# Kernel tuning notes

Hardware: AMD Instinct MI355X
Metric: run time of the kernel (lower is better)

## Reference

```python
import jax, jax.numpy as jnp
import numpy as np

N = 100_000   # nodes
R = 8         # relations (edge types)
E = 100_000   # edges per relation
D_IN = 64
D_OUT = 64


def setup_inputs() -> dict:
    key = jax.random.key(0)
    k1, k2, k3, k4 = jax.random.split(key, 4)
    feat = jax.random.normal(k1, (N, D_IN), dtype=jnp.float32)
    # per-relation weight matrices (nn.ParameterDict in the original)
    weight = jax.random.normal(k2, (R, D_IN, D_OUT), dtype=jnp.float32) / np.sqrt(D_IN).astype(np.float32)
    edge_src = jax.random.randint(k3, (R, E), 0, N)
    edge_dst = jax.random.randint(k4, (R, E), 0, N)
    return {"feat": feat, "weight": weight, "edge_src": edge_src, "edge_dst": edge_dst}


def reference(feat, weight, edge_src, edge_dst):
    # Per-relation: gather src features, dense matmul with that relation's
    # weight, scatter-sum messages into destination nodes; 'sum' across
    # relations (cross-type reducer) collapses into one big scatter-add.
    n = feat.shape[0]
    gathered = feat[edge_src]                            # [R, E, d_in] irregular gather
    msg = jnp.einsum('red,rdf->ref', gathered, weight)   # [R, E, d_out]
    out = jax.ops.segment_sum(
        msg.reshape(-1, msg.shape[-1]),                  # [R*E, d_out]
        edge_dst.reshape(-1),
        num_segments=n,
    )                                                    # [N, d_out]
    return out
```

## Files before the change

### kernel.cpp

```cpp
#include <hip/hip_runtime.h>
#include <hip/hip_bf16.h>


#define WAVES_PER_BLOCK 4
#define EDGES_PER_WAVE 64
#define TILE_E (WAVES_PER_BLOCK * EDGES_PER_WAVE)

__global__ __launch_bounds__(256) void rgcn_edge_kernel(
    const float* __restrict__ feat,
    const float* __restrict__ weight,
    const int*   __restrict__ esrc,
    const int*   __restrict__ edst,
    float*       __restrict__ out,
    int E, int blocksPerRel)
{
    const int t    = threadIdx.x;
    const int wave = t >> 6;
    const int lane = t & 63;

    const int r       = blockIdx.x / blocksPerRel;
    const int tileIdx = blockIdx.x % blocksPerRel;
    const int e0      = tileIdx * TILE_E + wave * EDGES_PER_WAVE;
    if (e0 >= E) return;

    const float* wbase = weight + (size_t)r * 4096 + lane;
    float wreg[64];
    #pragma unroll
    for (int d = 0; d < 64; ++d) wreg[d] = wbase[(size_t)d * 64];

    const int nE = min(EDGES_PER_WAVE, E - e0);
    const int ei = e0 + min(lane, nE - 1);
    const int sv = esrc[(size_t)r * E + ei];
    const int dv = edst[(size_t)r * E + ei];

    float* outl = out + lane;

    for (int i = 0; i < nE; ++i) {
        const int srow = __builtin_amdgcn_readlane(sv, i);
        const int drow = __builtin_amdgcn_readlane(dv, i);

        const float4* xp = (const float4*)(feat + (size_t)srow * 64);
        float a0 = 0.f, a1 = 0.f, a2 = 0.f, a3 = 0.f;
        #pragma unroll
        for (int c = 0; c < 16; ++c) {
            const float4 v = xp[c];
            a0 = fmaf(v.x, wreg[4 * c + 0], a0);
            a1 = fmaf(v.y, wreg[4 * c + 1], a1);
            a2 = fmaf(v.z, wreg[4 * c + 2], a2);
            a3 = fmaf(v.w, wreg[4 * c + 3], a3);
        }
        const float acc = (a0 + a1) + (a2 + a3);

        atomicAdd(outl + (size_t)drow * 64, acc);
    }
}

extern "C" void kernel_launch(void* const* d_in, const int* in_sizes, int n_in,
                              void* d_out, int out_size, void* d_ws, size_t ws_size,
                              hipStream_t stream) {
    const float* feat   = (const float*)d_in[0];
    const float* weight = (const float*)d_in[1];
    const int*   esrc   = (const int*)d_in[2];
    const int*   edst   = (const int*)d_in[3];
    float*       out    = (float*)d_out;

    const int R = in_sizes[1] / (64 * 64);
    const int E = in_sizes[2] / R;

    hipMemsetAsync(d_out, 0, (size_t)out_size * sizeof(float), stream);

    const int blocksPerRel = (E + TILE_E - 1) / TILE_E;
    const dim3 grid(R * blocksPerRel);
    const dim3 block(WAVES_PER_BLOCK * 64);
    rgcn_edge_kernel<<<grid, block, 0, stream>>>(feat, weight, esrc, edst, out,
                                                 E, blocksPerRel);
}
```

Baseline: 263.9 us.

## Bucket edges by destination block and accumulate messages in shared memory

```diff
diff --git a/kernel.cpp b/kernel.cpp
--- a/kernel.cpp
+++ b/kernel.cpp
@@ -2,43 +2,143 @@
 #include <hip/hip_bf16.h>
 
 
-#define WAVES_PER_BLOCK 4
-#define EDGES_PER_WAVE 64
-#define TILE_E (WAVES_PER_BLOCK * EDGES_PER_WAVE)
+#define BUCKET_SHIFT 7
+#define BUCKET_NODES 128
+#define REL_SHIFT 20
 
-__global__ __launch_bounds__(256) void rgcn_edge_kernel(
-    const float* __restrict__ feat,
-    const float* __restrict__ weight,
-    const int*   __restrict__ esrc,
-    const int*   __restrict__ edst,
-    float*       __restrict__ out,
-    int E, int blocksPerRel)
+__global__ __launch_bounds__(256) void k_hist(
+    const int* __restrict__ edst, unsigned* __restrict__ hist, int E, int R)
 {
-    const int t    = threadIdx.x;
-    const int wave = t >> 6;
-    const int lane = t & 63;
+    const int e = blockIdx.x * 256 + threadIdx.x;
+    const int r = blockIdx.y;
+    if (e < E) {
+        const unsigned d = (unsigned)edst[(size_t)r * E + e];
+        atomicAdd(&hist[(d >> BUCKET_SHIFT) * R + r], 1u);
+    }
+}
 
-    const int r       = blockIdx.x / blocksPerRel;
-    const int tileIdx = blockIdx.x % blocksPerRel;
-    const int e0      = tileIdx * TILE_E + wave * EDGES_PER_WAVE;
+__global__ __launch_bounds__(256) void k_scan(
+    const unsigned* __restrict__ hist, unsigned* __restrict__ base,
+    unsigned* __restrict__ cursor, int nbins)
+{
+    __shared__ unsigned psum[256];
+    const int t  = threadIdx.x;
+    const int C  = (nbins + 255) / 256;
+    const int i0 = t * C, i1 = min(i0 + C, nbins);
+    unsigned s = 0;
+    for (int i = i0; i < i1; ++i) s += hist[i];
+    psum[t] = s;
+    __syncthreads();
+    if (t == 0) {
+        unsigned run = 0;
+        for (int i = 0; i < 256; ++i) { unsigned v = psum[i]; psum[i] = run; run += v; }
+        base[nbins] = run;
+    }
+    __syncthreads();
+    unsigned run = psum[t];
+    for (int i = i0; i < i1; ++i) { base[i] = run; cursor[i] = run; run += hist[i]; }
+}
+
+__global__ __launch_bounds__(256) void k_scatter(
+    const int* __restrict__ esrc, const int* __restrict__ edst,
+    unsigned* __restrict__ cursor, uint2* __restrict__ rec, int E, int R)
+{
+    const int e = blockIdx.x * 256 + threadIdx.x;
+    const int r = blockIdx.y;
+    if (e < E) {
+        const size_t idx  = (size_t)r * E + e;
+        const unsigned d  = (unsigned)edst[idx];
+        const unsigned bin  = (d >> BUCKET_SHIFT) * R + r;
+        const unsigned slot = atomicAdd(&cursor[bin], 1u);
+        rec[slot] = make_uint2((unsigned)esrc[idx], d | ((unsigned)r << REL_SHIFT));
+    }
+}
+
+__global__ __launch_bounds__(256) void k_compute(
+    const float* __restrict__ feat, const float* __restrict__ weight,
+    const uint2* __restrict__ rec, const unsigned* __restrict__ base,
+    float* __restrict__ out, int N, int R)
+{
+    __shared__ float acc[BUCKET_NODES * 64];
+    const int t = threadIdx.x, wave = t >> 6, lane = t & 63;
+    const int b = blockIdx.x;
+
+    for (int i = t; i < BUCKET_NODES * 16; i += 256)
+        ((float4*)acc)[i] = make_float4(0.f, 0.f, 0.f, 0.f);
+    __syncthreads();
+
+    const unsigned s0 = base[(size_t)b * R];
+    const unsigned s1 = base[(size_t)(b + 1) * R];
+
+    float wreg[64];
+    int rcur = -1;
+
+    for (unsigned chunk = s0 + (unsigned)wave * 64u; chunk < s1; chunk += 256u) {
+        const int n = (int)min(64u, s1 - chunk);
+        const uint2 rv = rec[chunk + (unsigned)min(lane, n - 1)];
+        const unsigned myrel = (rv.y >> REL_SHIFT) & 7u;
+        int i = 0;
+        while (i < n) {
+            const int r = (__builtin_amdgcn_readlane((int)rv.y, i) >> REL_SHIFT) & 7;
+            unsigned long long neq = __ballot(myrel != (unsigned)r) >> i;
+            int run = neq ? (int)__builtin_ctzll(neq) : (n - i);
+            run = min(run, n - i);
+            if (r != rcur) {
+                const float* wb = weight + (size_t)r * 4096 + lane;
+                #pragma unroll
+                for (int d = 0; d < 64; ++d) wreg[d] = wb[(size_t)d * 64];
+                rcur = r;
+            }
+            const int jend = i + run;
+            for (int j = i; j < jend; ++j) {
+                const int srow = __builtin_amdgcn_readlane((int)rv.x, j);
+                const int dloc = __builtin_amdgcn_readlane((int)rv.y, j) & (BUCKET_NODES - 1);
+                const float4* xp = (const float4*)(feat + (size_t)srow * 64);
+                float a0 = 0.f, a1 = 0.f, a2 = 0.f, a3 = 0.f;
+                #pragma unroll
+                for (int c = 0; c < 16; ++c) {
+                    const float4 v = xp[c];
+                    a0 = fmaf(v.x, wreg[4 * c + 0], a0);
+                    a1 = fmaf(v.y, wreg[4 * c + 1], a1);
+                    a2 = fmaf(v.z, wreg[4 * c + 2], a2);
+                    a3 = fmaf(v.w, wreg[4 * c + 3], a3);
+                }
+                atomicAdd(&acc[dloc * 64 + lane], (a0 + a1) + (a2 + a3));
+            }
+            i = jend;
+        }
+    }
+
+    __syncthreads();
+    const int n0 = b << BUCKET_SHIFT;
+    for (int i = t; i < BUCKET_NODES * 16; i += 256) {
+        const int row = i >> 4;
+        if (n0 + row < N)
+            ((float4*)(out + (size_t)(n0 + row) * 64))[i & 15] = ((float4*)acc)[i];
+    }
+}
+
+#define FB_TILE_E 256
+__global__ __launch_bounds__(256) void k_fallback(
+    const float* __restrict__ feat, const float* __restrict__ weight,
+    const int* __restrict__ esrc, const int* __restrict__ edst,
+    float* __restrict__ out, int E, int blocksPerRel)
+{
+    const int t = threadIdx.x, wave = t >> 6, lane = t & 63;
+    const int r = blockIdx.x / blocksPerRel;
+    const int e0 = (blockIdx.x % blocksPerRel) * FB_TILE_E + wave * 64;
     if (e0 >= E) return;
-
     const float* wbase = weight + (size_t)r * 4096 + lane;
     float wreg[64];
     #pragma unroll
     for (int d = 0; d < 64; ++d) wreg[d] = wbase[(size_t)d * 64];
-
-    const int nE = min(EDGES_PER_WAVE, E - e0);
+    const int nE = min(64, E - e0);
     const int ei = e0 + min(lane, nE - 1);
     const int sv = esrc[(size_t)r * E + ei];
     const int dv = edst[(size_t)r * E + ei];
-
-    float* outl = out + lane;
-
     for (int i = 0; i < nE; ++i) {
         const int srow = __builtin_amdgcn_readlane(sv, i);
         const int drow = __builtin_amdgcn_readlane(dv, i);
-
         const float4* xp = (const float4*)(feat + (size_t)srow * 64);
         float a0 = 0.f, a1 = 0.f, a2 = 0.f, a3 = 0.f;
         #pragma unroll
@@ -49,9 +149,7 @@
             a2 = fmaf(v.z, wreg[4 * c + 2], a2);
             a3 = fmaf(v.w, wreg[4 * c + 3], a3);
         }
-        const float acc = (a0 + a1) + (a2 + a3);
-
-        atomicAdd(outl + (size_t)drow * 64, acc);
+        atomicAdd(out + (size_t)drow * 64 + lane, (a0 + a1) + (a2 + a3));
     }
 }
 
@@ -64,14 +162,34 @@
     const int*   edst   = (const int*)d_in[3];
     float*       out    = (float*)d_out;
 
-    const int R = in_sizes[1] / (64 * 64);
+    const int R = in_sizes[1] / 4096;
     const int E = in_sizes[2] / R;
+    const int N = in_sizes[0] / 64;
+    const size_t RE = (size_t)R * E;
+    const int NB    = (N + BUCKET_NODES - 1) / BUCKET_NODES;
+    const int NBINS = NB * R;
 
-    hipMemsetAsync(d_out, 0, (size_t)out_size * sizeof(float), stream);
+    const size_t recBytes  = RE * sizeof(uint2);
+    const size_t metaBytes = (size_t)(3 * NBINS + 2) * sizeof(unsigned);
 
-    const int blocksPerRel = (E + TILE_E - 1) / TILE_E;
-    const dim3 grid(R * blocksPerRel);
-    const dim3 block(WAVES_PER_BLOCK * 64);
-    rgcn_edge_kernel<<<grid, block, 0, stream>>>(feat, weight, esrc, edst, out,
-                                                 E, blocksPerRel);
+    if (ws_size < recBytes + metaBytes) {
+        hipMemsetAsync(d_out, 0, (size_t)out_size * sizeof(float), stream);
+        const int blocksPerRel = (E + FB_TILE_E - 1) / FB_TILE_E;
+        k_fallback<<<dim3(R * blocksPerRel), 256, 0, stream>>>(
+            feat, weight, esrc, edst, out, E, blocksPerRel);
+        return;
+    }
+
+    uint2*    rec    = (uint2*)d_ws;
+    unsigned* hist   = (unsigned*)((char*)d_ws + recBytes);
+    unsigned* basep  = hist + NBINS;
+    unsigned* cursor = basep + NBINS + 1;
+
+    hipMemsetAsync(hist, 0, (size_t)NBINS * sizeof(unsigned), stream);
+
+    const dim3 eg((E + 255) / 256, R);
+    k_hist   <<<eg, 256, 0, stream>>>(edst, hist, E, R);
+    k_scan   <<<1, 256, 0, stream>>>(hist, basep, cursor, NBINS);
+    k_scatter<<<eg, 256, 0, stream>>>(esrc, edst, cursor, rec, E, R);
+    k_compute<<<NB, 256, 0, stream>>>(feat, weight, rec, basep, out, N, R);
 }
```

Result: slower. 532.3 us (+101.7%).
